# Optimization experiments

Measured on AMD Instinct MI355X. Metric: run time of the kernel, lower is better.

Reference implementation:

```python
import jax, jax.numpy as jnp
import numpy as np

N = 65536
INPUT_DIM = 4
HIDDEN = 256
OUT_DIM = 64
NUM_FREQS = 10
NUM_LAYERS = 4  # -> 3 residual blocks
NUM_COMPOSE = 4
DIN_PE = INPUT_DIM + 2 * INPUT_DIM * NUM_FREQS  # 84


def setup_inputs() -> dict:
    key = jax.random.key(0)
    ks = jax.random.split(key, 10)
    x = jax.random.uniform(ks[0], (N, INPUT_DIM), jnp.float32, 0.1, 1.0)
    in_dim = jax.random.uniform(ks[1], (N,), jnp.float32, 0.5, 1.5)
    layer_id = jax.random.randint(ks[2], (N,), 0, NUM_COMPOSE, dtype=jnp.int32)
    s0 = 1.0 / np.sqrt(DIN_PE)
    sh = 1.0 / np.sqrt(HIDDEN)
    W0 = jax.random.normal(ks[3], (NUM_COMPOSE, DIN_PE, HIDDEN), jnp.float32) * s0
    b0 = jax.random.normal(ks[4], (NUM_COMPOSE, HIDDEN), jnp.float32) * s0
    Wh = jax.random.normal(ks[5], (NUM_COMPOSE, NUM_LAYERS - 1, HIDDEN, HIDDEN), jnp.float32) * sh
    bh = jax.random.normal(ks[6], (NUM_COMPOSE, NUM_LAYERS - 1, HIDDEN), jnp.float32) * sh
    scal = jax.random.normal(ks[7], (NUM_COMPOSE, NUM_LAYERS - 1), jnp.float32) * 0.5
    Wout = jax.random.normal(ks[8], (NUM_COMPOSE, HIDDEN, OUT_DIM), jnp.float32) * sh
    bout = jax.random.normal(ks[9], (NUM_COMPOSE, OUT_DIM), jnp.float32) * sh
    return {"x": x, "in_dim": in_dim, "layer_id": layer_id, "W0": W0, "b0": b0,
            "Wh": Wh, "bh": bh, "scal": scal, "Wout": Wout, "bout": bout}


def _positional_encoding(x):
    # x: [N, D]; out order matches torch: [x, (sin,cos) for each freq i, each dim j]
    freqs = (2.0 ** jnp.arange(NUM_FREQS, dtype=x.dtype)) * np.pi  # [F]
    ang = x[:, None, :] * freqs[None, :, None]                      # [N, F, D]
    sc = jnp.stack([jnp.sin(ang), jnp.cos(ang)], axis=-1)           # [N, F, D, 2]
    return jnp.concatenate([x, sc.reshape(x.shape[0], -1)], axis=1)  # [N, D+2FD]


def reference(x, in_dim, layer_id, W0, b0, Wh, bh, scal, Wout, bout):
    # x[:, :3] = x[:, :3] / x[:, 3:]
    x = jnp.concatenate([x[:, :3] / x[:, 3:4], x[:, 3:]], axis=1)
    xe = _positional_encoding(x)  # [N, 84]

    def one_model(W0c, b0c, Whc, bhc, sc, Woutc, boutc):
        h = jax.nn.relu(xe @ W0c + b0c)           # [N, H]
        for k in range(NUM_LAYERS - 1):
            h = sc[k] * jax.nn.relu(h @ Whc[k] + bhc[k]) + h
        return h @ Woutc + boutc                  # [N, Dout]

    outs = jax.vmap(one_model)(W0, b0, Wh, bh, scal, Wout, bout)  # [C, N, Dout]
    # dispatch/combine: select each row's expert output
    out = jnp.take_along_axis(outs.transpose(1, 0, 2),
                              layer_id[:, None, None], axis=1)[:, 0]  # [N, Dout]
    return out / in_dim[:, None]
```

## Files before the change

kernel.cpp:

```cpp
#include <hip/hip_runtime.h>
#include <hip/hip_bf16.h>
#include <math.h>

#define N_ROWS 65536
#define H 256
#define DOUT 64
#define NC 4
#define NLAYERS_HIDDEN 3
#define DIN_PE 84
#define KPE 96
#define XE_STRIDE 104
#define BM 64
#define FB_STRIDE 68

#define CHUNK 512
#define WT0_PER_E (3 * 16 * CHUNK)
#define WTH_PER_L (8 * 16 * CHUNK)
#define WTOUT_PER_E (8 * 4 * CHUNK)

using bf16 = __hip_bfloat16;
typedef __bf16 bf16x8 __attribute__((ext_vector_type(8)));
typedef float f32x4 __attribute__((ext_vector_type(4)));

__global__ void bucket_kernel(const int* __restrict__ layer_id,
                              int* __restrict__ gcnt, int* __restrict__ idx) {
  __shared__ int lcnt[NC];
  __shared__ int lbase[NC];
  const int tid = threadIdx.x;
  if (tid < NC) lcnt[tid] = 0;
  __syncthreads();
  const int i = blockIdx.x * blockDim.x + tid;
  const int e = layer_id[i];
  const int lp = atomicAdd(&lcnt[e], 1);
  __syncthreads();
  if (tid < NC) lbase[tid] = atomicAdd(&gcnt[tid], lcnt[tid]);
  __syncthreads();
  idx[e * N_ROWS + lbase[e] + lp] = i;
}

__global__ void prep_weights(const float* __restrict__ W0,
                             const float* __restrict__ Wh,
                             const float* __restrict__ Wout,
                             bf16* __restrict__ wt0, bf16* __restrict__ wth,
                             bf16* __restrict__ wtout) {
  const int n0 = NC * WT0_PER_E;
  const int nh = NC * 3 * WTH_PER_L;
  const int no = NC * WTOUT_PER_E;
  const int total = n0 + nh + no;
  for (int i = blockIdx.x * blockDim.x + threadIdx.x; i < total;
       i += gridDim.x * blockDim.x) {
    if (i < n0) {
      int c = i / WT0_PER_E; int r = i % WT0_PER_E;
      int kbi = r / (16 * CHUNK); int r2 = r % (16 * CHUNK);
      int nblk = r2 / CHUNK; int w = r2 % CHUNK;
      int lane = w / 8, j = w % 8;
      int n = nblk * 16 + (lane & 15);
      int k = kbi * 32 + (lane >> 4) * 8 + j;
      float v = (k < DIN_PE) ? W0[(c * DIN_PE + k) * H + n] : 0.f;
      wt0[i] = __float2bfloat16(v);
    } else if (i < n0 + nh) {
      int u = i - n0;
      int cl = u / WTH_PER_L; int r = u % WTH_PER_L;
      int kbi = r / (16 * CHUNK); int r2 = r % (16 * CHUNK);
      int nblk = r2 / CHUNK; int w = r2 % CHUNK;
      int lane = w / 8, j = w % 8;
      int n = nblk * 16 + (lane & 15);
      int k = kbi * 32 + (lane >> 4) * 8 + j;
      wth[u] = __float2bfloat16(Wh[(cl * H + k) * H + n]);
    } else {
      int u = i - n0 - nh;
      int c = u / WTOUT_PER_E; int r = u % WTOUT_PER_E;
      int kbi = r / (4 * CHUNK); int r2 = r % (4 * CHUNK);
      int nblk = r2 / CHUNK; int w = r2 % CHUNK;
      int lane = w / 8, j = w % 8;
      int n = nblk * 16 + (lane & 15);
      int k = kbi * 32 + (lane >> 4) * 8 + j;
      wtout[u] = __float2bfloat16(Wout[(c * H + k) * DOUT + n]);
    }
  }
}

__global__ __launch_bounds__(256, 3) void mlp_kernel(
    const float* __restrict__ x, const float* __restrict__ in_dim,
    const int* __restrict__ gcnt, const int* __restrict__ idx,
    const bf16* __restrict__ wt0, const float* __restrict__ b0,
    const bf16* __restrict__ wth, const float* __restrict__ bh,
    const float* __restrict__ scal, const bf16* __restrict__ wtout,
    const float* __restrict__ bout, float* __restrict__ out) {
  const int bid = blockIdx.x;
  const int c0 = gcnt[0], c1 = gcnt[1], c2 = gcnt[2], c3 = gcnt[3];
  const int n0 = (c0 + 63) >> 6, n1 = (c1 + 63) >> 6, n2 = (c2 + 63) >> 6,
            n3 = (c3 + 63) >> 6;
  int e, tb, cnt;
  if (bid < n0) { e = 0; tb = bid; cnt = c0; }
  else if (bid < n0 + n1) { e = 1; tb = bid - n0; cnt = c1; }
  else if (bid < n0 + n1 + n2) { e = 2; tb = bid - n0 - n1; cnt = c2; }
  else if (bid < n0 + n1 + n2 + n3) { e = 3; tb = bid - n0 - n1 - n2; cnt = c3; }
  else return;
  const int base = tb * BM;

  __shared__ int ridx[BM];
  __shared__ float indim_s[BM];
  __shared__ __align__(16) char smem[BM * H * 2];
  bf16* xe = (bf16*)smem;
  bf16* hs = (bf16*)smem;
  float* fbuf = (float*)smem;

  const int tid = threadIdx.x;
  if (tid < BM) {
    int p = base + tid;
    int ri = (p < cnt) ? idx[e * N_ROWS + p] : -1;
    ridx[tid] = ri;
    indim_s[tid] = (ri >= 0) ? in_dim[ri] : 1.f;
  }
  __syncthreads();

  {
    const int r = tid >> 2, d = tid & 3;
    const int ri = ridx[r];
    float xd = 0.f, x3 = 1.f;
    if (ri >= 0) { xd = x[ri * 4 + d]; x3 = x[ri * 4 + 3]; }
    float v = (d < 3) ? (xd / x3) : x3;
    if (ri < 0) v = 0.f;
    bf16* row = xe + r * XE_STRIDE;
    row[d] = __float2bfloat16(v);
    float f = 3.14159265358979323846f;
#pragma unroll 1
    for (int q = 0; q < 10; ++q) {
      float sn, cs;
      __sincosf(v * f, &sn, &cs);
      row[4 + q * 8 + d * 2] = __float2bfloat16(sn);
      row[4 + q * 8 + d * 2 + 1] = __float2bfloat16(cs);
      f *= 2.f;
    }
#pragma unroll 1
    for (int c = DIN_PE + d; c < XE_STRIDE; c += 4) row[c] = __float2bfloat16(0.f);
  }
  __syncthreads();

  const int lane = tid & 63;
  const int wid = tid >> 6;
  const int l15 = lane & 15;
  const int lq = lane >> 4;
  const int wb = wid * 64;

  f32x4 acc[4][4];

  {
    const bf16* W = wt0 + (size_t)e * WT0_PER_E + lane * 8;
    const float* bias = b0 + e * H + wb;
#pragma unroll
    for (int it = 0; it < 4; ++it) {
      f32x4 bv = *(const f32x4*)(bias + it * 16 + lq * 4);
#pragma unroll
      for (int jt = 0; jt < 4; ++jt) acc[it][jt] = bv;
    }
#pragma unroll 1
    for (int kb = 0; kb < 3; ++kb) {
      bf16x8 aw[4], bx[4];
#pragma unroll
      for (int it = 0; it < 4; ++it)
        aw[it] = *(const bf16x8*)(W + (kb * 16 + wid * 4 + it) * CHUNK);
#pragma unroll
      for (int jt = 0; jt < 4; ++jt)
        bx[jt] = *(const bf16x8*)(xe + (jt * 16 + l15) * XE_STRIDE + kb * 32 + lq * 8);
#pragma unroll
      for (int it = 0; it < 4; ++it)
#pragma unroll
        for (int jt = 0; jt < 4; ++jt)
          acc[it][jt] = __builtin_amdgcn_mfma_f32_16x16x32_bf16(
              aw[it], bx[jt], acc[it][jt], 0, 0, 0);
    }
    __syncthreads();
#pragma unroll
    for (int it = 0; it < 4; ++it)
#pragma unroll
      for (int jt = 0; jt < 4; ++jt) {
        int m = jt * 16 + l15;
        int nb = wb + it * 16 + lq * 4;
        int byte = ((m * H + nb) * 2) ^ ((l15 & 7) << 4);
        bf16 neu[4];
#pragma unroll
        for (int r = 0; r < 4; ++r)
          neu[r] = __float2bfloat16(fmaxf(acc[it][jt][r], 0.f));
        *(ushort4*)((char*)hs + byte) = *(ushort4*)neu;
      }
  }
  __syncthreads();

#pragma unroll 1
  for (int l = 0; l < NLAYERS_HIDDEN; ++l) {
    const bf16* W = wth + (size_t)(e * 3 + l) * WTH_PER_L + lane * 8;
    const float* bias = bh + (e * 3 + l) * H + wb;
    const float sc = scal[e * 3 + l];
#pragma unroll
    for (int it = 0; it < 4; ++it) {
      f32x4 bv = *(const f32x4*)(bias + it * 16 + lq * 4);
#pragma unroll
      for (int jt = 0; jt < 4; ++jt) acc[it][jt] = bv;
    }
    bf16x8 aw0[4], aw1[4];
#pragma unroll
    for (int it = 0; it < 4; ++it)
      aw0[it] = *(const bf16x8*)(W + (wid * 4 + it) * CHUNK);
#pragma unroll 1
    for (int kb = 0; kb < 8; kb += 2) {
#pragma unroll
      for (int it = 0; it < 4; ++it)
        aw1[it] = *(const bf16x8*)(W + ((kb + 1) * 16 + wid * 4 + it) * CHUNK);
      {
        bf16x8 bx[4];
#pragma unroll
        for (int jt = 0; jt < 4; ++jt) {
          int m = jt * 16 + l15;
          int byte = ((m * H + kb * 32 + lq * 8) * 2) ^ ((l15 & 7) << 4);
          bx[jt] = *(const bf16x8*)((const char*)hs + byte);
        }
#pragma unroll
        for (int it = 0; it < 4; ++it)
#pragma unroll
          for (int jt = 0; jt < 4; ++jt)
            acc[it][jt] = __builtin_amdgcn_mfma_f32_16x16x32_bf16(
                aw0[it], bx[jt], acc[it][jt], 0, 0, 0);
      }
      {
        int kn = (kb + 2) & 7;
#pragma unroll
        for (int it = 0; it < 4; ++it)
          aw0[it] = *(const bf16x8*)(W + (kn * 16 + wid * 4 + it) * CHUNK);
        bf16x8 bx[4];
#pragma unroll
        for (int jt = 0; jt < 4; ++jt) {
          int m = jt * 16 + l15;
          int byte = ((m * H + (kb + 1) * 32 + lq * 8) * 2) ^ ((l15 & 7) << 4);
          bx[jt] = *(const bf16x8*)((const char*)hs + byte);
        }
#pragma unroll
        for (int it = 0; it < 4; ++it)
#pragma unroll
          for (int jt = 0; jt < 4; ++jt)
            acc[it][jt] = __builtin_amdgcn_mfma_f32_16x16x32_bf16(
                aw1[it], bx[jt], acc[it][jt], 0, 0, 0);
      }
    }
    __syncthreads();
#pragma unroll
    for (int it = 0; it < 4; ++it)
#pragma unroll
      for (int jt = 0; jt < 4; ++jt) {
        int m = jt * 16 + l15;
        int nb = wb + it * 16 + lq * 4;
        int byte = ((m * H + nb) * 2) ^ ((l15 & 7) << 4);
        ushort4* p = (ushort4*)((char*)hs + byte);
        bf16 old[4]; *(ushort4*)old = *p;
        bf16 neu[4];
#pragma unroll
        for (int r = 0; r < 4; ++r) {
          float hv = sc * fmaxf(acc[it][jt][r], 0.f) + __bfloat162float(old[r]);
          neu[r] = __float2bfloat16(hv);
        }
        *p = *(ushort4*)neu;
      }
    __syncthreads();
  }

  {
    const bf16* W = wtout + (size_t)e * WTOUT_PER_E + lane * 8;
    const float* bias = bout + e * DOUT + wid * 16;
    f32x4 facc[4];
    f32x4 bv = *(const f32x4*)(bias + lq * 4);
#pragma unroll
    for (int jt = 0; jt < 4; ++jt) facc[jt] = bv;
    bf16x8 aw0, aw1;
    aw0 = *(const bf16x8*)(W + wid * CHUNK);
#pragma unroll 1
    for (int kb = 0; kb < 8; kb += 2) {
      aw1 = *(const bf16x8*)(W + ((kb + 1) * 4 + wid) * CHUNK);
      {
        bf16x8 bx[4];
#pragma unroll
        for (int jt = 0; jt < 4; ++jt) {
          int m = jt * 16 + l15;
          int byte = ((m * H + kb * 32 + lq * 8) * 2) ^ ((l15 & 7) << 4);
          bx[jt] = *(const bf16x8*)((const char*)hs + byte);
        }
#pragma unroll
        for (int jt = 0; jt < 4; ++jt)
          facc[jt] = __builtin_amdgcn_mfma_f32_16x16x32_bf16(aw0, bx[jt], facc[jt], 0, 0, 0);
      }
      {
        int kn = (kb + 2) & 7;
        aw0 = *(const bf16x8*)(W + (kn * 4 + wid) * CHUNK);
        bf16x8 bx[4];
#pragma unroll
        for (int jt = 0; jt < 4; ++jt) {
          int m = jt * 16 + l15;
          int byte = ((m * H + (kb + 1) * 32 + lq * 8) * 2) ^ ((l15 & 7) << 4);
          bx[jt] = *(const bf16x8*)((const char*)hs + byte);
        }
#pragma unroll
        for (int jt = 0; jt < 4; ++jt)
          facc[jt] = __builtin_amdgcn_mfma_f32_16x16x32_bf16(aw1, bx[jt], facc[jt], 0, 0, 0);
      }
    }
    __syncthreads();
#pragma unroll
    for (int jt = 0; jt < 4; ++jt) {
      int m = jt * 16 + l15;
      *(f32x4*)(fbuf + m * FB_STRIDE + wid * 16 + lq * 4) = facc[jt];
    }
  }
  __syncthreads();

#pragma unroll 1
  for (int p = 0; p < 4; ++p) {
    int item = p * 256 + tid;
    int row = item >> 4;
    int ch = item & 15;
    int ri = ridx[row];
    if (ri >= 0) {
      f32x4 v = *(const f32x4*)(fbuf + row * FB_STRIDE + ch * 4);
      float inv = indim_s[row];
      v[0] /= inv; v[1] /= inv; v[2] /= inv; v[3] /= inv;
      *(f32x4*)(out + (size_t)ri * DOUT + ch * 4) = v;
    }
  }
}

extern "C" void kernel_launch(void* const* d_in, const int* in_sizes, int n_in,
                              void* d_out, int out_size, void* d_ws,
                              size_t ws_size, hipStream_t stream) {
  const float* x = (const float*)d_in[0];
  const float* in_dim = (const float*)d_in[1];
  const int* layer_id = (const int*)d_in[2];
  const float* W0 = (const float*)d_in[3];
  const float* b0 = (const float*)d_in[4];
  const float* Wh = (const float*)d_in[5];
  const float* bh = (const float*)d_in[6];
  const float* scal = (const float*)d_in[7];
  const float* Wout = (const float*)d_in[8];
  const float* bout = (const float*)d_in[9];
  float* out = (float*)d_out;

  char* ws = (char*)d_ws;
  int* gcnt = (int*)ws;
  int* idx = (int*)(ws + 16);
  bf16* wt0 = (bf16*)(ws + 16 + (size_t)NC * N_ROWS * 4);
  bf16* wth = wt0 + NC * WT0_PER_E;
  bf16* wtout = wth + NC * 3 * WTH_PER_L;

  hipMemsetAsync(gcnt, 0, NC * sizeof(int), stream);
  bucket_kernel<<<N_ROWS / 256, 256, 0, stream>>>(layer_id, gcnt, idx);
  prep_weights<<<512, 256, 0, stream>>>(W0, Wh, Wout, wt0, wth, wtout);
  mlp_kernel<<<N_ROWS / BM + NC - 1, 256, 0, stream>>>(
      x, in_dim, gcnt, idx, wt0, b0, wth, bh, scal, wtout, bout, out);
}
```

Before: 144.6 us.

## Prefetch whole next-layer weight tile into registers during current layer epilogue

Holds a full layer's per-wave weight fragments in registers (aw[8][4], 128 VGPRs). Each layer's weights are issued as global loads before the epilogue and barrier of the previous layer, so their latency overlaps the LDS writeback and sync instead of sitting inside the k-loop. The first layer's weights are loaded before the positional-encoding stage. In exchange, occupancy drops from 3 to 2 waves per EU through amdgpu_waves_per_eu, and register pressure rises with a spill risk.

Result: slower. 160.8 us (+11.2%).

```diff
diff --git a/kernel.cpp b/kernel.cpp
--- a/kernel.cpp
+++ b/kernel.cpp
@@ -80,7 +80,9 @@
   }
 }
 
-__global__ __launch_bounds__(256, 3) void mlp_kernel(
+__global__ __attribute__((amdgpu_flat_work_group_size(256, 256),
+                          amdgpu_waves_per_eu(2, 2)))
+void mlp_kernel(
     const float* __restrict__ x, const float* __restrict__ in_dim,
     const int* __restrict__ gcnt, const int* __restrict__ idx,
     const bf16* __restrict__ wt0, const float* __restrict__ b0,
@@ -99,6 +101,24 @@
   else return;
   const int base = tb * BM;
 
+  const int tid = threadIdx.x;
+  const int lane = tid & 63;
+  const int wid = tid >> 6;
+  const int l15 = lane & 15;
+  const int lq = lane >> 4;
+  const int wb = wid * 64;
+
+  bf16x8 aw[8][4];
+
+  {
+    const bf16* W = wt0 + (size_t)e * WT0_PER_E + lane * 8;
+#pragma unroll
+    for (int kb = 0; kb < 3; ++kb)
+#pragma unroll
+      for (int it = 0; it < 4; ++it)
+        aw[kb][it] = *(const bf16x8*)(W + (kb * 16 + wid * 4 + it) * CHUNK);
+  }
+
   __shared__ int ridx[BM];
   __shared__ float indim_s[BM];
   __shared__ __align__(16) char smem[BM * H * 2];
@@ -106,7 +126,6 @@
   bf16* hs = (bf16*)smem;
   float* fbuf = (float*)smem;
 
-  const int tid = threadIdx.x;
   if (tid < BM) {
     int p = base + tid;
     int ri = (p < cnt) ? idx[e * N_ROWS + p] : -1;
@@ -138,16 +157,9 @@
   }
   __syncthreads();
 
-  const int lane = tid & 63;
-  const int wid = tid >> 6;
-  const int l15 = lane & 15;
-  const int lq = lane >> 4;
-  const int wb = wid * 64;
-
   f32x4 acc[4][4];
 
   {
-    const bf16* W = wt0 + (size_t)e * WT0_PER_E + lane * 8;
     const float* bias = b0 + e * H + wb;
 #pragma unroll
     for (int it = 0; it < 4; ++it) {
@@ -155,12 +167,9 @@
 #pragma unroll
       for (int jt = 0; jt < 4; ++jt) acc[it][jt] = bv;
     }
-#pragma unroll 1
+#pragma unroll
     for (int kb = 0; kb < 3; ++kb) {
-      bf16x8 aw[4], bx[4];
-#pragma unroll
-      for (int it = 0; it < 4; ++it)
-        aw[it] = *(const bf16x8*)(W + (kb * 16 + wid * 4 + it) * CHUNK);
+      bf16x8 bx[4];
 #pragma unroll
       for (int jt = 0; jt < 4; ++jt)
         bx[jt] = *(const bf16x8*)(xe + (jt * 16 + l15) * XE_STRIDE + kb * 32 + lq * 8);
@@ -169,7 +178,15 @@
 #pragma unroll
         for (int jt = 0; jt < 4; ++jt)
           acc[it][jt] = __builtin_amdgcn_mfma_f32_16x16x32_bf16(
-              aw[it], bx[jt], acc[it][jt], 0, 0, 0);
+              aw[kb][it], bx[jt], acc[it][jt], 0, 0, 0);
+    }
+    {
+      const bf16* Wn = wth + (size_t)(e * 3 + 0) * WTH_PER_L + lane * 8;
+#pragma unroll
+      for (int kb = 0; kb < 8; ++kb)
+#pragma unroll
+        for (int it = 0; it < 4; ++it)
+          aw[kb][it] = *(const bf16x8*)(Wn + (kb * 16 + wid * 4 + it) * CHUNK);
     }
     __syncthreads();
 #pragma unroll
@@ -190,7 +207,6 @@
 
 #pragma unroll 1
   for (int l = 0; l < NLAYERS_HIDDEN; ++l) {
-    const bf16* W = wth + (size_t)(e * 3 + l) * WTH_PER_L + lane * 8;
     const float* bias = bh + (e * 3 + l) * H + wb;
     const float sc = scal[e * 3 + l];
 #pragma unroll
@@ -199,49 +215,34 @@
 #pragma unroll
       for (int jt = 0; jt < 4; ++jt) acc[it][jt] = bv;
     }
-    bf16x8 aw0[4], aw1[4];
-#pragma unroll
-    for (int it = 0; it < 4; ++it)
-      aw0[it] = *(const bf16x8*)(W + (wid * 4 + it) * CHUNK);
-#pragma unroll 1
-    for (int kb = 0; kb < 8; kb += 2) {
+#pragma unroll
+    for (int kb = 0; kb < 8; ++kb) {
+      bf16x8 bx[4];
+#pragma unroll
+      for (int jt = 0; jt < 4; ++jt) {
+        int m = jt * 16 + l15;
+        int byte = ((m * H + kb * 32 + lq * 8) * 2) ^ ((l15 & 7) << 4);
+        bx[jt] = *(const bf16x8*)((const char*)hs + byte);
+      }
 #pragma unroll
       for (int it = 0; it < 4; ++it)
-        aw1[it] = *(const bf16x8*)(W + ((kb + 1) * 16 + wid * 4 + it) * CHUNK);
-      {
-        bf16x8 bx[4];
-#pragma unroll
-        for (int jt = 0; jt < 4; ++jt) {
-          int m = jt * 16 + l15;
-          int byte = ((m * H + kb * 32 + lq * 8) * 2) ^ ((l15 & 7) << 4);
-          bx[jt] = *(const bf16x8*)((const char*)hs + byte);
-        }
+#pragma unroll
+        for (int jt = 0; jt < 4; ++jt)
+          acc[it][jt] = __builtin_amdgcn_mfma_f32_16x16x32_bf16(
+              aw[kb][it], bx[jt], acc[it][jt], 0, 0, 0);
+    }
+    if (l < NLAYERS_HIDDEN - 1) {
+      const bf16* Wn = wth + (size_t)(e * 3 + l + 1) * WTH_PER_L + lane * 8;
+#pragma unroll
+      for (int kb = 0; kb < 8; ++kb)
 #pragma unroll
         for (int it = 0; it < 4; ++it)
-#pragma unroll
-          for (int jt = 0; jt < 4; ++jt)
-            acc[it][jt] = __builtin_amdgcn_mfma_f32_16x16x32_bf16(
-                aw0[it], bx[jt], acc[it][jt], 0, 0, 0);
-      }
-      {
-        int kn = (kb + 2) & 7;
-#pragma unroll
-        for (int it = 0; it < 4; ++it)
-          aw0[it] = *(const bf16x8*)(W + (kn * 16 + wid * 4 + it) * CHUNK);
-        bf16x8 bx[4];
-#pragma unroll
-        for (int jt = 0; jt < 4; ++jt) {
-          int m = jt * 16 + l15;
-          int byte = ((m * H + (kb + 1) * 32 + lq * 8) * 2) ^ ((l15 & 7) << 4);
-          bx[jt] = *(const bf16x8*)((const char*)hs + byte);
-        }
-#pragma unroll
-        for (int it = 0; it < 4; ++it)
-#pragma unroll
-          for (int jt = 0; jt < 4; ++jt)
-            acc[it][jt] = __builtin_amdgcn_mfma_f32_16x16x32_bf16(
-                aw1[it], bx[jt], acc[it][jt], 0, 0, 0);
-      }
+          aw[kb][it] = *(const bf16x8*)(Wn + (kb * 16 + wid * 4 + it) * CHUNK);
+    } else {
+      const bf16* Wn = wtout + (size_t)e * WTOUT_PER_E + lane * 8;
+#pragma unroll
+      for (int kb = 0; kb < 8; ++kb)
+        aw[kb][0] = *(const bf16x8*)(Wn + (kb * 4 + wid) * CHUNK);
     }
     __syncthreads();
 #pragma unroll
@@ -265,43 +266,24 @@
   }
 
   {
-    const bf16* W = wtout + (size_t)e * WTOUT_PER_E + lane * 8;
     const float* bias = bout + e * DOUT + wid * 16;
     f32x4 facc[4];
     f32x4 bv = *(const f32x4*)(bias + lq * 4);
 #pragma unroll
     for (int jt = 0; jt < 4; ++jt) facc[jt] = bv;
-    bf16x8 aw0, aw1;
-    aw0 = *(const bf16x8*)(W + wid * CHUNK);
-#pragma unroll 1
-    for (int kb = 0; kb < 8; kb += 2) {
-      aw1 = *(const bf16x8*)(W + ((kb + 1) * 4 + wid) * CHUNK);
-      {
-        bf16x8 bx[4];
-#pragma unroll
-        for (int jt = 0; jt < 4; ++jt) {
-          int m = jt * 16 + l15;
-          int byte = ((m * H + kb * 32 + lq * 8) * 2) ^ ((l15 & 7) << 4);
-          bx[jt] = *(const bf16x8*)((const char*)hs + byte);
-        }
-#pragma unroll
-        for (int jt = 0; jt < 4; ++jt)
-          facc[jt] = __builtin_amdgcn_mfma_f32_16x16x32_bf16(aw0, bx[jt], facc[jt], 0, 0, 0);
+#pragma unroll
+    for (int kb = 0; kb < 8; ++kb) {
+      bf16x8 bx[4];
+#pragma unroll
+      for (int jt = 0; jt < 4; ++jt) {
+        int m = jt * 16 + l15;
+        int byte = ((m * H + kb * 32 + lq * 8) * 2) ^ ((l15 & 7) << 4);
+        bx[jt] = *(const bf16x8*)((const char*)hs + byte);
       }
-      {
-        int kn = (kb + 2) & 7;
-        aw0 = *(const bf16x8*)(W + (kn * 4 + wid) * CHUNK);
-        bf16x8 bx[4];
-#pragma unroll
-        for (int jt = 0; jt < 4; ++jt) {
-          int m = jt * 16 + l15;
-          int byte = ((m * H + (kb + 1) * 32 + lq * 8) * 2) ^ ((l15 & 7) << 4);
-          bx[jt] = *(const bf16x8*)((const char*)hs + byte);
-        }
-#pragma unroll
-        for (int jt = 0; jt < 4; ++jt)
-          facc[jt] = __builtin_amdgcn_mfma_f32_16x16x32_bf16(aw1, bx[jt], facc[jt], 0, 0, 0);
-      }
+#pragma unroll
+      for (int jt = 0; jt < 4; ++jt)
+        facc[jt] = __builtin_amdgcn_mfma_f32_16x16x32_bf16(
+            aw[kb][0], bx[jt], facc[jt], 0, 0, 0);
     }
     __syncthreads();
 #pragma unroll
```
